# Kernel optimization log

Hardware: AMD Instinct MI355X
Metric: run time of the kernel (lower is better)

The kernel has to match this reference:

```python
import jax, jax.numpy as jnp
import numpy as np

EMB = 1024

def setup_inputs() -> dict:
    key = jax.random.key(0)
    ks = jax.random.split(key, 7)
    s = 1.0 / np.sqrt(EMB)
    x = jax.random.normal(ks[0], (4, 2048, EMB), dtype=jnp.float32)
    Wk = jax.random.normal(ks[1], (EMB, EMB), dtype=jnp.float32) * s
    bk = jnp.zeros((EMB,), dtype=jnp.float32)
    Wq = jax.random.normal(ks[2], (EMB, EMB), dtype=jnp.float32) * s
    bq = jnp.zeros((EMB,), dtype=jnp.float32)
    Wv = jax.random.normal(ks[3], (EMB, EMB), dtype=jnp.float32) * s
    bv = jnp.zeros((EMB,), dtype=jnp.float32)
    return {"x": x, "Wk": Wk, "bk": bk, "Wq": Wq, "bq": bq, "Wv": Wv, "bv": bv}

def reference(x, Wk, bk, Wq, bq, Wv, bv):
    # Linear layers: x @ W.T + b (torch nn.Linear convention)
    k = jnp.einsum('bse,fe->bsf', x, Wk) + bk
    q = jnp.einsum('bse,fe->bsf', x, Wq) + bq
    v = jnp.einsum('bse,fe->bsf', x, Wv) + bv
    E = x.shape[-1]
    # NOTE: original computes k @ q^T (not q @ k^T) — reproduce faithfully.
    sim = jnp.einsum('bsd,btd->bst', k, q) / jnp.sqrt(jnp.float32(E))
    S = x.shape[1]
    causal = jnp.tril(jnp.ones((S, S), dtype=bool))  # [S,S]
    sim = jnp.where(causal, sim, -jnp.inf)
    attn = jax.nn.softmax(sim, axis=-1)
    return jnp.einsum('bst,btd->bsd', attn, v)
```

## Files before the change

### kernel.cpp

```cpp
#include <hip/hip_runtime.h>
#include <cstdint>


typedef __attribute__((ext_vector_type(8))) _Float16 f16x8;
typedef __attribute__((ext_vector_type(4))) float f32x4;

__device__ __forceinline__ unsigned short f2h(float x) {
  return __builtin_bit_cast(unsigned short, (_Float16)x);
}

__device__ __forceinline__ void lds_dma16(const void* g, void* l) {
  auto gp = reinterpret_cast<const __attribute__((address_space(1))) void*>(
      reinterpret_cast<uintptr_t>(g));
  auto lp = reinterpret_cast<__attribute__((address_space(3))) void*>(
      reinterpret_cast<uintptr_t>(l));
  __builtin_amdgcn_global_load_lds(gp, lp, 16, 0, 0);
}

__device__ __forceinline__ void stage_half(const unsigned short* __restrict__ G,
                                           int ld, unsigned short* lds,
                                           int tid) {
  const int r = tid >> 3;
  const int c = ((tid & 7) ^ (r & 7)) * 8;
  lds_dma16(G + (size_t)r * ld + c, lds + tid * 8);
  lds_dma16(G + (size_t)(r + 64) * ld + c, lds + 4096 + tid * 8);
}

__device__ __forceinline__ void g256_iter(
    const unsigned short* __restrict__ Ag, const unsigned short* __restrict__ Bg,
    int lda, int ldb, unsigned short* As, unsigned short* Bs,
    f32x4 (&acc)[2][2][2][4], int k0, bool last) {
  const int tid = threadIdx.x;
  const int lane = tid & 63, wave = tid >> 6;
  const int qwm = wave >> 1, qwn = wave & 1;
  const int rr = lane & 15, qq = lane >> 4;
  const int arow = (qwm * 32 + rr) * 64;
  const int brow = (qwn * 64 + rr) * 64;
  const int s7 = rr & 7;
  const int soff0 = (qq ^ s7) * 8;
  const int soff1 = ((4 + qq) ^ s7) * 8;

#pragma unroll
  for (int p = 0; p < 8; ++p) {
    const int buf = p >> 2, qm = (p >> 1) & 1, qn = p & 1;
    const unsigned short* Ar = As + buf * 16384 + qm * 8192 + arow;
    const unsigned short* Br = Bs + buf * 16384 + qn * 8192 + brow;
    f16x8 af[2][2], bf[4][2];
#pragma unroll
    for (int fi = 0; fi < 2; ++fi) {
      af[fi][0] = *(const f16x8*)(Ar + fi * 1024 + soff0);
      af[fi][1] = *(const f16x8*)(Ar + fi * 1024 + soff1);
    }
#pragma unroll
    for (int fj = 0; fj < 4; ++fj) {
      bf[fj][0] = *(const f16x8*)(Br + fj * 1024 + soff0);
      bf[fj][1] = *(const f16x8*)(Br + fj * 1024 + soff1);
    }

    if (p == 0) {
      stage_half(Ag + (size_t)128 * lda + (k0 + 64), lda, As + 24576, tid);
    } else if (p == 1) {
      stage_half(Bg + (size_t)128 * ldb + (k0 + 64), ldb, Bs + 24576, tid);
    } else if (!last) {
      if (p == 2)      stage_half(Ag + (k0 + 128), lda, As, tid);
      else if (p == 3) stage_half(Bg + (k0 + 128), ldb, Bs, tid);
      else if (p == 4) stage_half(Ag + (size_t)128 * lda + (k0 + 128), lda, As + 8192, tid);
      else if (p == 5) stage_half(Bg + (size_t)128 * ldb + (k0 + 128), ldb, Bs + 8192, tid);
      else if (p == 6) stage_half(Ag + (k0 + 192), lda, As + 16384, tid);
      else             stage_half(Bg + (k0 + 192), ldb, Bs + 16384, tid);
    }

    asm volatile("s_waitcnt lgkmcnt(8)" ::: "memory");
    __builtin_amdgcn_s_barrier();
    asm volatile("s_waitcnt lgkmcnt(0)" ::: "memory");
    __builtin_amdgcn_sched_barrier(0);
    __builtin_amdgcn_s_setprio(1);
#pragma unroll
    for (int h = 0; h < 2; ++h)
#pragma unroll
      for (int fi = 0; fi < 2; ++fi)
#pragma unroll
        for (int fj = 0; fj < 4; ++fj)
          acc[qm][qn][fi][fj] = __builtin_amdgcn_mfma_f32_16x16x32_f16(
              af[fi][h], bf[fj][h], acc[qm][qn][fi][fj], 0, 0, 0);
    __builtin_amdgcn_s_setprio(0);
    if (p == 3) {
      if (last) asm volatile("s_waitcnt vmcnt(0)" ::: "memory");
      else      asm volatile("s_waitcnt vmcnt(4)" ::: "memory");
    } else if (p == 7 && !last) {
      asm volatile("s_waitcnt vmcnt(4)" ::: "memory");
    }
    __builtin_amdgcn_s_barrier();
  }
}

__device__ __forceinline__ void gemm256(
    const unsigned short* __restrict__ Ag, const unsigned short* __restrict__ Bg,
    int lda, int ldb, int nk, unsigned short* As, unsigned short* Bs,
    f32x4 (&acc)[2][2][2][4]) {
  const int tid = threadIdx.x;
#pragma unroll
  for (int a = 0; a < 2; ++a)
#pragma unroll
    for (int b = 0; b < 2; ++b)
#pragma unroll
      for (int c = 0; c < 2; ++c)
#pragma unroll
      for (int d = 0; d < 4; ++d) {
        f32x4 z = {0.f, 0.f, 0.f, 0.f};
        acc[a][b][c][d] = z;
      }

  stage_half(Ag, lda, As, tid);
  stage_half(Ag + (size_t)128 * lda, lda, As + 8192, tid);
  stage_half(Bg, ldb, Bs, tid);
  stage_half(Bg + (size_t)128 * ldb, ldb, Bs + 8192, tid);
  stage_half(Ag + 64, lda, As + 16384, tid);
  stage_half(Bg + 64, ldb, Bs + 16384, tid);
  asm volatile("s_waitcnt vmcnt(4)" ::: "memory");
  __builtin_amdgcn_s_barrier();

  const int NIT = nk >> 7;
  for (int it = 0; it < NIT - 1; ++it)
    g256_iter(Ag, Bg, lda, ldb, As, Bs, acc, it << 7, false);
  g256_iter(Ag, Bg, lda, ldb, As, Bs, acc, (NIT - 1) << 7, true);
}

__device__ __forceinline__ void gemm128_k64(
    const unsigned short* __restrict__ Ag, const unsigned short* __restrict__ Bg,
    int lda, int ldb, int nk, unsigned short* As, unsigned short* Bs,
    f32x4 acc[4][4]) {
  const int tid = threadIdx.x;
  const int lane = tid & 63, wave = tid >> 6;
  const int wm = wave >> 1, wn = wave & 1;
  const int sr = lane >> 3;
  const int scb = ((lane & 7) ^ sr) * 8;
  const int rr = lane & 15, qq = lane >> 4;
  const int slot0 = ((qq) ^ (rr & 7)) * 8;
  const int slot1 = ((4 + qq) ^ (rr & 7)) * 8;

#pragma unroll
  for (int i = 0; i < 4; ++i)
#pragma unroll
    for (int j = 0; j < 4; ++j) {
      f32x4 z = {0.f, 0.f, 0.f, 0.f};
      acc[i][j] = z;
    }

#pragma unroll
  for (int c = 0; c < 4; ++c) {
    int chunk = wave * 4 + c;
    int row = chunk * 8 + sr;
    lds_dma16(Ag + (size_t)row * lda + scb, As + chunk * 512);
    lds_dma16(Bg + (size_t)row * ldb + scb, Bs + chunk * 512);
  }

  int buf = 0;
  for (int k0 = 0; k0 < nk; k0 += 64) {
    __syncthreads();
    const int kn = k0 + 64;
    if (kn < nk) {
      unsigned short* An = As + (buf ^ 1) * 8192;
      unsigned short* Bn = Bs + (buf ^ 1) * 8192;
#pragma unroll
      for (int c = 0; c < 4; ++c) {
        int chunk = wave * 4 + c;
        int row = chunk * 8 + sr;
        lds_dma16(Ag + (size_t)row * lda + kn + scb, An + chunk * 512);
        lds_dma16(Bg + (size_t)row * ldb + kn + scb, Bn + chunk * 512);
      }
    }

    const unsigned short* Ar = As + buf * 8192 + (wm * 64 + rr) * 64;
    const unsigned short* Br = Bs + buf * 8192 + (wn * 64 + rr) * 64;
    {
      f16x8 af[4], bf[4];
#pragma unroll
      for (int i = 0; i < 4; ++i) af[i] = *(const f16x8*)(Ar + i * 1024 + slot0);
#pragma unroll
      for (int j = 0; j < 4; ++j) bf[j] = *(const f16x8*)(Br + j * 1024 + slot0);
#pragma unroll
      for (int i = 0; i < 4; ++i)
#pragma unroll
        for (int j = 0; j < 4; ++j)
          acc[i][j] = __builtin_amdgcn_mfma_f32_16x16x32_f16(af[i], bf[j],
                                                             acc[i][j], 0, 0, 0);
    }
    {
      f16x8 af[4], bf[4];
#pragma unroll
      for (int i = 0; i < 4; ++i) af[i] = *(const f16x8*)(Ar + i * 1024 + slot1);
#pragma unroll
      for (int j = 0; j < 4; ++j) bf[j] = *(const f16x8*)(Br + j * 1024 + slot1);
#pragma unroll
      for (int i = 0; i < 4; ++i)
#pragma unroll
        for (int j = 0; j < 4; ++j)
          acc[i][j] = __builtin_amdgcn_mfma_f32_16x16x32_f16(af[i], bf[j],
                                                             acc[i][j], 0, 0, 0);
    }
    buf ^= 1;
  }
}

__global__ void cvt_kernel(const float* __restrict__ x,
                           const float* __restrict__ w0,
                           const float* __restrict__ w1,
                           const float* __restrict__ w2,
                           unsigned short* __restrict__ dst,
                           float* __restrict__ rsum) {
  int i = blockIdx.x * 256 + threadIdx.x;
  if (i >= 2883584) {
    int z2 = i - 2883584;
    float4 z = {0.f, 0.f, 0.f, 0.f};
    ((float4*)rsum)[z2] = z;
    return;
  }
  const float* s;
  size_t si;
  if (i < 2097152) {
    s = x; si = i;
  } else {
    int j = i - 2097152;
    int z = j >> 18;
    s = (z == 0) ? w0 : ((z == 1) ? w1 : w2);
    si = j & 262143;
  }
  float4 f = ((const float4*)s)[si];
  ushort4 u;
  u.x = f2h(f.x); u.y = f2h(f.y); u.z = f2h(f.z); u.w = f2h(f.w);
  ((ushort4*)dst)[i] = u;
}

__global__ __launch_bounds__(512, 2) void qkv256_kernel(
    const unsigned short* __restrict__ xh, const unsigned short* __restrict__ wh,
    const float* __restrict__ bk, const float* __restrict__ bq,
    const float* __restrict__ bv, unsigned short* __restrict__ kh,
    unsigned short* __restrict__ qh, unsigned short* __restrict__ vT) {
  __shared__ unsigned short As[32768], Bs[32768];
  const int job = (blockIdx.x & 7) * 48 + (blockIdx.x >> 3);

  const unsigned short* Ag;
  const unsigned short* Bg;
  if (job < 256) {
    const int tm = job >> 3, tn = job & 7;
    Ag = xh + (size_t)tm * 256 * 1024;
    Bg = wh + (size_t)tn * 256 * 1024;
  } else {
    const int j = job - 256;
    const int dt = j >> 5, tt = j & 31;
    Ag = wh + 2097152 + (size_t)dt * 256 * 1024;
    Bg = xh + (size_t)tt * 256 * 1024;
  }

  f32x4 acc[2][2][2][4];
  gemm256(Ag, Bg, 1024, 1024, 1024, As, Bs, acc);

  const int tid = threadIdx.x;
  const int lane = tid & 63, wave = tid >> 6;
  const int qwm = wave >> 1, qwn = wave & 1, rr = lane & 15, qq = lane >> 4;

  if (job < 256) {
    const int tm = job >> 3, tn = job & 7;
    const bool isq = tn >= 4;
    unsigned short* dst = isq ? qh : kh;
    const float* bias = isq ? bq : bk;
    const int nbase = (tn & 3) * 256;
    float bj[2][4];
#pragma unroll
    for (int qn = 0; qn < 2; ++qn)
#pragma unroll
      for (int fj = 0; fj < 4; ++fj)
        bj[qn][fj] = bias[nbase + qn * 128 + qwn * 64 + fj * 16 + rr];
#pragma unroll
    for (int qm = 0; qm < 2; ++qm)
#pragma unroll
      for (int fi = 0; fi < 2; ++fi)
#pragma unroll
        for (int reg = 0; reg < 4; ++reg) {
          const int m = tm * 256 + qm * 128 + qwm * 32 + fi * 16 + qq * 4 + reg;
#pragma unroll
          for (int qn = 0; qn < 2; ++qn)
#pragma unroll
            for (int fj = 0; fj < 4; ++fj) {
              const int n = nbase + qn * 128 + qwn * 64 + fj * 16 + rr;
              dst[(size_t)m * 1024 + n] =
                  f2h(acc[qm][qn][fi][fj][reg] + bj[qn][fj]);
            }
        }
  } else {
    const int j = job - 256;
    const int dt = j >> 5, tt = j & 31;
#pragma unroll
    for (int qm = 0; qm < 2; ++qm)
#pragma unroll
      for (int fi = 0; fi < 2; ++fi) {
        const int d0 = dt * 256 + qm * 128 + qwm * 32 + fi * 16 + qq * 4;
        const float4 b4 = *(const float4*)(bv + d0);
        const float bir[4] = {b4.x, b4.y, b4.z, b4.w};
#pragma unroll
        for (int reg = 0; reg < 4; ++reg) {
          const int d = d0 + reg;
#pragma unroll
          for (int qn = 0; qn < 2; ++qn)
#pragma unroll
            for (int fj = 0; fj < 4; ++fj) {
              const int tg = tt * 256 + qn * 128 + qwn * 64 + fj * 16 + rr;
              const int bb = tg >> 11, t = tg & 2047;
              vT[((size_t)(bb * 1024 + d)) * 2048 + t] =
                  f2h(acc[qm][qn][fi][fj][reg] + bir[reg]);
            }
        }
      }
  }
}

__global__ __launch_bounds__(256) void scores_kernel(
    const unsigned short* __restrict__ kh, const unsigned short* __restrict__ qh,
    unsigned short* __restrict__ P, float* __restrict__ rsum) {
  const int b = blockIdx.y;
  int idx = blockIdx.x;
  int ts = (int)((sqrtf(8.0f * idx + 1.0f) - 1.0f) * 0.5f);
  while ((ts + 1) * (ts + 2) / 2 <= idx) ++ts;
  while (ts * (ts + 1) / 2 > idx) --ts;
  const int tt = idx - ts * (ts + 1) / 2;
  __shared__ unsigned short As[2 * 128 * 64], Bs[2 * 128 * 64];

  f32x4 acc[4][4];
  gemm128_k64(kh + ((size_t)(b * 2048 + ts * 128)) * 1024,
              qh + ((size_t)(b * 2048 + tt * 128)) * 1024,
              1024, 1024, 1024, As, Bs, acc);

  const int lane = threadIdx.x & 63, wave = threadIdx.x >> 6;
  const int wm = wave >> 1, wn = wave & 1, rr = lane & 15, qq = lane >> 4;
  unsigned short* Pb = P + (size_t)b * 2048 * 2048;
  float* rs = rsum + b * 2048;
#pragma unroll
  for (int i = 0; i < 4; ++i)
#pragma unroll
    for (int reg = 0; reg < 4; ++reg) {
      int srow = ts * 128 + wm * 64 + i * 16 + qq * 4 + reg;
      float p = 0.f;
#pragma unroll
      for (int j = 0; j < 4; ++j) {
        int tcol = tt * 128 + wn * 64 + j * 16 + rr;
        float e = (tcol <= srow) ? __expf(acc[i][j][reg] * 0.03125f - 4.0f)
                                 : 0.0f;
        Pb[(size_t)srow * 2048 + tcol] = f2h(e);
        p += e;
      }
#pragma unroll
      for (int off = 1; off < 16; off <<= 1) p += __shfl_xor(p, off);
      if (rr == 0) atomicAdd(rs + srow, p);
    }
}

__global__ __launch_bounds__(256) void pv_gemm_kernel(
    const unsigned short* __restrict__ P, const unsigned short* __restrict__ vT,
    const float* __restrict__ rsum, float* __restrict__ out) {
  const int td = blockIdx.x, ts = 15 - blockIdx.y, b = blockIdx.z;
  __shared__ unsigned short As[2 * 128 * 64], Bs[2 * 128 * 64];

  f32x4 acc[4][4];
  gemm128_k64(P + ((size_t)(b * 2048 + ts * 128)) * 2048,
              vT + ((size_t)(b * 1024 + td * 128)) * 2048,
              2048, 2048, (ts + 1) * 128, As, Bs, acc);

  const int lane = threadIdx.x & 63, wave = threadIdx.x >> 6;
  const int wm = wave >> 1, wn = wave & 1, rr = lane & 15, qq = lane >> 4;
#pragma unroll
  for (int i = 0; i < 4; ++i) {
    int s0 = ts * 128 + wm * 64 + i * 16 + qq * 4;
    float4 r4 = *(const float4*)(rsum + b * 2048 + s0);
    float rv[4] = {__builtin_amdgcn_rcpf(r4.x), __builtin_amdgcn_rcpf(r4.y),
                   __builtin_amdgcn_rcpf(r4.z), __builtin_amdgcn_rcpf(r4.w)};
#pragma unroll
    for (int reg = 0; reg < 4; ++reg) {
      int srow = s0 + reg;
#pragma unroll
      for (int j = 0; j < 4; ++j) {
        int dcol = td * 128 + wn * 64 + j * 16 + rr;
        out[((size_t)(b * 2048 + srow)) * 1024 + dcol] =
            acc[i][j][reg] * rv[reg];
      }
    }
  }
}

extern "C" void kernel_launch(void* const* d_in, const int* in_sizes, int n_in,
                              void* d_out, int out_size, void* d_ws,
                              size_t ws_size, hipStream_t stream) {
  const float* x  = (const float*)d_in[0];
  const float* Wk = (const float*)d_in[1];
  const float* bk = (const float*)d_in[2];
  const float* Wq = (const float*)d_in[3];
  const float* bq = (const float*)d_in[4];
  const float* Wv = (const float*)d_in[5];
  const float* bv = (const float*)d_in[6];
  float* out = (float*)d_out;

  char* ws = (char*)d_ws;
  const size_t MB = 1ull << 20;
  unsigned short* xh = (unsigned short*)(ws + 0);
  unsigned short* wh = (unsigned short*)(ws + 16 * MB);
  unsigned short* P  = (unsigned short*)(ws + 0);
  unsigned short* kh = (unsigned short*)(ws + 38 * MB);
  unsigned short* qh = (unsigned short*)(ws + 54 * MB);
  unsigned short* vT = (unsigned short*)(ws + 70 * MB);
  float* rsum = (float*)(ws + 86 * MB);

  cvt_kernel<<<11272, 256, 0, stream>>>(x, Wk, Wq, Wv, xh, rsum);
  qkv256_kernel<<<384, 512, 0, stream>>>(xh, wh, bk, bq, bv, kh, qh, vT);
  scores_kernel<<<dim3(136, 4), 256, 0, stream>>>(kh, qh, P, rsum);
  pv_gemm_kernel<<<dim3(8, 16, 4), 256, 0, stream>>>(P, vT, rsum, out);
}
```

Measured before the change: 244.7 us.

## Restructure projection GEMM to 2x4 wave grid with 128x64 per-wave tiles

The 256x256 projection GEMM changes its wave decomposition from quadrant-based 32x64 subtiles over four passes to a 2x4 wave grid. Each wave now owns a 128x64 output block and loads 8 A and 4 B fragments per K=32 phase. The staging schedule is also reorganised: it prefetches whole 64-wide K halves per phase and waits with vmcnt(0) instead of partial counts. The aim is fewer LDS reads per MFMA and a simpler pipeline, at the cost of less overlap of global loads with compute and possibly more register pressure.

```diff
diff --git a/kernel.cpp b/kernel.cpp
--- a/kernel.cpp
+++ b/kernel.cpp
@@ -26,104 +26,83 @@
   lds_dma16(G + (size_t)(r + 64) * ld + c, lds + 4096 + tid * 8);
 }
 
-__device__ __forceinline__ void g256_iter(
+__device__ __forceinline__ void gemm256(
     const unsigned short* __restrict__ Ag, const unsigned short* __restrict__ Bg,
-    int lda, int ldb, unsigned short* As, unsigned short* Bs,
-    f32x4 (&acc)[2][2][2][4], int k0, bool last) {
+    int lda, int ldb, int nk, unsigned short* As, unsigned short* Bs,
+    f32x4 (&acc)[8][4]) {
   const int tid = threadIdx.x;
   const int lane = tid & 63, wave = tid >> 6;
-  const int qwm = wave >> 1, qwn = wave & 1;
+  const int wr = wave >> 2, wc = wave & 3;
   const int rr = lane & 15, qq = lane >> 4;
-  const int arow = (qwm * 32 + rr) * 64;
-  const int brow = (qwn * 64 + rr) * 64;
   const int s7 = rr & 7;
   const int soff0 = (qq ^ s7) * 8;
   const int soff1 = ((4 + qq) ^ s7) * 8;
-
-#pragma unroll
-  for (int p = 0; p < 8; ++p) {
-    const int buf = p >> 2, qm = (p >> 1) & 1, qn = p & 1;
-    const unsigned short* Ar = As + buf * 16384 + qm * 8192 + arow;
-    const unsigned short* Br = Bs + buf * 16384 + qn * 8192 + brow;
-    f16x8 af[2][2], bf[4][2];
-#pragma unroll
-    for (int fi = 0; fi < 2; ++fi) {
-      af[fi][0] = *(const f16x8*)(Ar + fi * 1024 + soff0);
-      af[fi][1] = *(const f16x8*)(Ar + fi * 1024 + soff1);
-    }
+  const int aoff = wr * 8192 + rr * 64;
+  const int boff = (wc >> 1) * 8192 + (wc & 1) * 4096 + rr * 64;
+
+#pragma unroll
+  for (int fi = 0; fi < 8; ++fi)
 #pragma unroll
     for (int fj = 0; fj < 4; ++fj) {
-      bf[fj][0] = *(const f16x8*)(Br + fj * 1024 + soff0);
-      bf[fj][1] = *(const f16x8*)(Br + fj * 1024 + soff1);
-    }
-
-    if (p == 0) {
-      stage_half(Ag + (size_t)128 * lda + (k0 + 64), lda, As + 24576, tid);
-    } else if (p == 1) {
-      stage_half(Bg + (size_t)128 * ldb + (k0 + 64), ldb, Bs + 24576, tid);
-    } else if (!last) {
-      if (p == 2)      stage_half(Ag + (k0 + 128), lda, As, tid);
-      else if (p == 3) stage_half(Bg + (k0 + 128), ldb, Bs, tid);
-      else if (p == 4) stage_half(Ag + (size_t)128 * lda + (k0 + 128), lda, As + 8192, tid);
-      else if (p == 5) stage_half(Bg + (size_t)128 * ldb + (k0 + 128), ldb, Bs + 8192, tid);
-      else if (p == 6) stage_half(Ag + (k0 + 192), lda, As + 16384, tid);
-      else             stage_half(Bg + (k0 + 192), ldb, Bs + 16384, tid);
-    }
-
-    asm volatile("s_waitcnt lgkmcnt(8)" ::: "memory");
-    __builtin_amdgcn_s_barrier();
-    asm volatile("s_waitcnt lgkmcnt(0)" ::: "memory");
-    __builtin_amdgcn_sched_barrier(0);
-    __builtin_amdgcn_s_setprio(1);
-#pragma unroll
-    for (int h = 0; h < 2; ++h)
-#pragma unroll
-      for (int fi = 0; fi < 2; ++fi)
-#pragma unroll
-        for (int fj = 0; fj < 4; ++fj)
-          acc[qm][qn][fi][fj] = __builtin_amdgcn_mfma_f32_16x16x32_f16(
-              af[fi][h], bf[fj][h], acc[qm][qn][fi][fj], 0, 0, 0);
-    __builtin_amdgcn_s_setprio(0);
-    if (p == 3) {
-      if (last) asm volatile("s_waitcnt vmcnt(0)" ::: "memory");
-      else      asm volatile("s_waitcnt vmcnt(4)" ::: "memory");
-    } else if (p == 7 && !last) {
-      asm volatile("s_waitcnt vmcnt(4)" ::: "memory");
-    }
-    __builtin_amdgcn_s_barrier();
-  }
-}
-
-__device__ __forceinline__ void gemm256(
-    const unsigned short* __restrict__ Ag, const unsigned short* __restrict__ Bg,
-    int lda, int ldb, int nk, unsigned short* As, unsigned short* Bs,
-    f32x4 (&acc)[2][2][2][4]) {
-  const int tid = threadIdx.x;
-#pragma unroll
-  for (int a = 0; a < 2; ++a)
-#pragma unroll
-    for (int b = 0; b < 2; ++b)
-#pragma unroll
-      for (int c = 0; c < 2; ++c)
-#pragma unroll
-      for (int d = 0; d < 4; ++d) {
-        f32x4 z = {0.f, 0.f, 0.f, 0.f};
-        acc[a][b][c][d] = z;
-      }
+      f32x4 z = {0.f, 0.f, 0.f, 0.f};
+      acc[fi][fj] = z;
+    }
 
   stage_half(Ag, lda, As, tid);
   stage_half(Ag + (size_t)128 * lda, lda, As + 8192, tid);
   stage_half(Bg, ldb, Bs, tid);
   stage_half(Bg + (size_t)128 * ldb, ldb, Bs + 8192, tid);
-  stage_half(Ag + 64, lda, As + 16384, tid);
-  stage_half(Bg + 64, ldb, Bs + 16384, tid);
-  asm volatile("s_waitcnt vmcnt(4)" ::: "memory");
+  asm volatile("s_waitcnt vmcnt(0)" ::: "memory");
   __builtin_amdgcn_s_barrier();
 
-  const int NIT = nk >> 7;
-  for (int it = 0; it < NIT - 1; ++it)
-    g256_iter(Ag, Bg, lda, ldb, As, Bs, acc, it << 7, false);
-  g256_iter(Ag, Bg, lda, ldb, As, Bs, acc, (NIT - 1) << 7, true);
+  for (int k0 = 0; k0 < nk; k0 += 128) {
+    const bool last = (k0 + 128 >= nk);
+#pragma unroll
+    for (int P = 0; P < 4; ++P) {
+      const int b = P >> 1;
+      if (P == 0) {
+        stage_half(Ag + (k0 + 64), lda, As + 16384, tid);
+        stage_half(Ag + (size_t)128 * lda + (k0 + 64), lda, As + 24576, tid);
+      } else if (P == 1) {
+        stage_half(Bg + (k0 + 64), ldb, Bs + 16384, tid);
+        stage_half(Bg + (size_t)128 * ldb + (k0 + 64), ldb, Bs + 24576, tid);
+      } else if (!last) {
+        if (P == 2) {
+          stage_half(Ag + (k0 + 128), lda, As, tid);
+          stage_half(Ag + (size_t)128 * lda + (k0 + 128), lda, As + 8192, tid);
+        } else {
+          stage_half(Bg + (k0 + 128), ldb, Bs, tid);
+          stage_half(Bg + (size_t)128 * ldb + (k0 + 128), ldb, Bs + 8192, tid);
+        }
+      }
+      const int so = (P & 1) ? soff1 : soff0;
+      const unsigned short* Ar = As + b * 16384 + aoff + so;
+      const unsigned short* Br = Bs + b * 16384 + boff + so;
+      f16x8 af[8], bf[4];
+#pragma unroll
+      for (int fi = 0; fi < 8; ++fi) af[fi] = *(const f16x8*)(Ar + fi * 1024);
+#pragma unroll
+      for (int fj = 0; fj < 4; ++fj) bf[fj] = *(const f16x8*)(Br + fj * 1024);
+      asm volatile("s_waitcnt lgkmcnt(8)" ::: "memory");
+      __builtin_amdgcn_s_barrier();
+      asm volatile("s_waitcnt lgkmcnt(0)" ::: "memory");
+      __builtin_amdgcn_sched_barrier(0);
+      __builtin_amdgcn_s_setprio(1);
+#pragma unroll
+      for (int fi = 0; fi < 8; ++fi)
+#pragma unroll
+        for (int fj = 0; fj < 4; ++fj)
+          acc[fi][fj] = __builtin_amdgcn_mfma_f32_16x16x32_f16(
+              af[fi], bf[fj], acc[fi][fj], 0, 0, 0);
+      __builtin_amdgcn_s_setprio(0);
+      if (P == 1) {
+        asm volatile("s_waitcnt vmcnt(0)" ::: "memory");
+      } else if (P == 3 && !last) {
+        asm volatile("s_waitcnt vmcnt(0)" ::: "memory");
+      }
+      __builtin_amdgcn_s_barrier();
+    }
+  }
 }
 
 __device__ __forceinline__ void gemm128_k64(
@@ -253,12 +232,12 @@
     Bg = xh + (size_t)tt * 256 * 1024;
   }
 
-  f32x4 acc[2][2][2][4];
+  f32x4 acc[8][4];
   gemm256(Ag, Bg, 1024, 1024, 1024, As, Bs, acc);
 
   const int tid = threadIdx.x;
   const int lane = tid & 63, wave = tid >> 6;
-  const int qwm = wave >> 1, qwn = wave & 1, rr = lane & 15, qq = lane >> 4;
+  const int wr = wave >> 2, wc = wave & 3, rr = lane & 15, qq = lane >> 4;
 
   if (job < 256) {
     const int tm = job >> 3, tn = job & 7;
@@ -266,52 +245,41 @@
     unsigned short* dst = isq ? qh : kh;
     const float* bias = isq ? bq : bk;
     const int nbase = (tn & 3) * 256;
-    float bj[2][4];
-#pragma unroll
-    for (int qn = 0; qn < 2; ++qn)
-#pragma unroll
-      for (int fj = 0; fj < 4; ++fj)
-        bj[qn][fj] = bias[nbase + qn * 128 + qwn * 64 + fj * 16 + rr];
-#pragma unroll
-    for (int qm = 0; qm < 2; ++qm)
-#pragma unroll
-      for (int fi = 0; fi < 2; ++fi)
-#pragma unroll
-        for (int reg = 0; reg < 4; ++reg) {
-          const int m = tm * 256 + qm * 128 + qwm * 32 + fi * 16 + qq * 4 + reg;
-#pragma unroll
-          for (int qn = 0; qn < 2; ++qn)
-#pragma unroll
-            for (int fj = 0; fj < 4; ++fj) {
-              const int n = nbase + qn * 128 + qwn * 64 + fj * 16 + rr;
-              dst[(size_t)m * 1024 + n] =
-                  f2h(acc[qm][qn][fi][fj][reg] + bj[qn][fj]);
-            }
+    float bj[4];
+#pragma unroll
+    for (int fj = 0; fj < 4; ++fj)
+      bj[fj] = bias[nbase + wc * 64 + fj * 16 + rr];
+#pragma unroll
+    for (int fi = 0; fi < 8; ++fi)
+#pragma unroll
+      for (int reg = 0; reg < 4; ++reg) {
+        const int m = tm * 256 + wr * 128 + fi * 16 + qq * 4 + reg;
+#pragma unroll
+        for (int fj = 0; fj < 4; ++fj) {
+          const int n = nbase + wc * 64 + fj * 16 + rr;
+          dst[(size_t)m * 1024 + n] = f2h(acc[fi][fj][reg] + bj[fj]);
         }
+      }
   } else {
     const int j = job - 256;
     const int dt = j >> 5, tt = j & 31;
 #pragma unroll
-    for (int qm = 0; qm < 2; ++qm)
-#pragma unroll
-      for (int fi = 0; fi < 2; ++fi) {
-        const int d0 = dt * 256 + qm * 128 + qwm * 32 + fi * 16 + qq * 4;
-        const float4 b4 = *(const float4*)(bv + d0);
-        const float bir[4] = {b4.x, b4.y, b4.z, b4.w};
-#pragma unroll
-        for (int reg = 0; reg < 4; ++reg) {
-          const int d = d0 + reg;
-#pragma unroll
-          for (int qn = 0; qn < 2; ++qn)
-#pragma unroll
-            for (int fj = 0; fj < 4; ++fj) {
-              const int tg = tt * 256 + qn * 128 + qwn * 64 + fj * 16 + rr;
-              const int bb = tg >> 11, t = tg & 2047;
-              vT[((size_t)(bb * 1024 + d)) * 2048 + t] =
-                  f2h(acc[qm][qn][fi][fj][reg] + bir[reg]);
-            }
+    for (int fi = 0; fi < 8; ++fi) {
+      const int d0 = dt * 256 + wr * 128 + fi * 16 + qq * 4;
+      const float4 b4 = *(const float4*)(bv + d0);
+      const float bir[4] = {b4.x, b4.y, b4.z, b4.w};
+#pragma unroll
+      for (int reg = 0; reg < 4; ++reg) {
+        const int d = d0 + reg;
+#pragma unroll
+        for (int fj = 0; fj < 4; ++fj) {
+          const int tg = tt * 256 + wc * 64 + fj * 16 + rr;
+          const int bb = tg >> 11, t = tg & 2047;
+          vT[((size_t)(bb * 1024 + d)) * 2048 + t] =
+              f2h(acc[fi][fj][reg] + bir[reg]);
         }
       }
+    }
   }
 }
 
```

After: 244.5 us. No clear change (-0.1%).
